# Kernel tuning notes

Measured on AMD Instinct MI355X. Metric: run time of the kernel, lower is better.

## Reference

```python
import jax, jax.numpy as jnp
import numpy as np

CURV = 0.9            # geoopt PoincareBall(0.9)
SQRT_C = CURV ** 0.5
MIN_NORM = 1e-15
PROJ_EPS = 4e-3       # geoopt float32 boundary eps
ATANH_EPS = 1e-7
COS_EPS = 1e-8        # torch.cosine_similarity eps


def _norm(x):
    return jnp.sqrt(jnp.maximum(jnp.sum(x * x, axis=-1, keepdims=True), MIN_NORM * MIN_NORM))


def _project(x):
    # project onto ball of radius (1-eps)/sqrt(c)
    n = jnp.maximum(_norm(x), MIN_NORM)
    maxnorm = (1.0 - PROJ_EPS) / SQRT_C
    return jnp.where(n > maxnorm, x / n * maxnorm, x)


def expmap0(u):
    n = jnp.maximum(_norm(u), MIN_NORM)
    gamma = jnp.tanh(SQRT_C * n) * u / (SQRT_C * n)
    return _project(gamma)


def mobius_add(x, y):
    c = CURV
    x2 = jnp.sum(x * x, axis=-1, keepdims=True)
    y2 = jnp.sum(y * y, axis=-1, keepdims=True)
    xy = jnp.sum(x * y, axis=-1, keepdims=True)
    num = (1.0 + 2.0 * c * xy + c * y2) * x + (1.0 - c * x2) * y
    den = 1.0 + 2.0 * c * xy + c * c * x2 * y2
    return num / jnp.maximum(den, MIN_NORM)


def pdist(x, y):
    # dist(x,y) = 2/sqrt(c) * artanh(sqrt(c) * ||(-x) (+) y||)
    d = mobius_add(-x, y)
    n = _norm(d)[..., 0]
    z = jnp.clip(SQRT_C * n, -1.0 + ATANH_EPS, 1.0 - ATANH_EPS)
    return 2.0 / SQRT_C * jnp.arctanh(z)


def cos_sim(a, b):
    na = jnp.maximum(jnp.sqrt(jnp.sum(a * a, axis=-1)), COS_EPS)
    nb = jnp.maximum(jnp.sqrt(jnp.sum(b * b, axis=-1)), COS_EPS)
    return jnp.sum(a * b, axis=-1) / (na * nb)


def setup_inputs() -> dict:
    key = jax.random.key(0)
    ks = jax.random.split(key, 11)
    B, L, Ls, C, Lc, H, R = 4, 512, 128, 20, 128, 768, 512
    s = 0.02  # keep projected embeddings in a realistic range
    return {
        "text_out": jax.random.normal(ks[0], (B, L, H), jnp.float32),
        "summary_out": jax.random.normal(ks[1], (B, Ls, H), jnp.float32),
        "candidate_out": jax.random.normal(ks[2], (B, C, Lc, H), jnp.float32),
        "W_d": jax.random.normal(ks[3], (H, R), jnp.float32) * s,
        "W_s": jax.random.normal(ks[4], (H, R), jnp.float32) * s,
        "W_c": jax.random.normal(ks[5], (H, R), jnp.float32) * s,
        "W_p": jax.random.normal(ks[6], (R, R), jnp.float32) * s,
        "conv_w1": jax.random.normal(ks[7], (1, H, R), jnp.float32) * s,
        "conv_b1": jax.random.normal(ks[8], (R,), jnp.float32) * s,
        "conv_w2": jax.random.normal(ks[9], (2, H, R), jnp.float32) * s,
        "conv_b2": jax.random.normal(ks[10], (R,), jnp.float32) * s,
    }


def _forward(text_out, summary_out, candidate_out, W_d, W_s, W_c, W_p,
             conv_w1, conv_b1, conv_w2, conv_b2):
    # --- document ---
    doc_emb = expmap0(text_out[:, 0, :] @ W_d)                       # [B,R]

    # NGramers (max_gram=2, eval mode so dropout is identity)
    x = text_out[:, 1:-1, :]                                         # [B,L-2,H]
    y1 = jax.nn.relu(jnp.einsum('blh,hr->blr', x, conv_w1[0]) + conv_b1)
    y2 = jax.nn.relu(jnp.einsum('blh,hr->blr', x[:, :-1], conv_w2[0])
                     + jnp.einsum('blh,hr->blr', x[:, 1:], conv_w2[1]) + conv_b2)
    gram = jnp.concatenate([y1, y2], axis=1)                         # [B,2L-5,R]

    doc_word_emb = expmap0(jnp.einsum('blr,rk->blk', gram, W_p))     # [B,T,R]
    doc_inter = 1.0 / pdist(doc_word_emb, doc_emb[:, None, :])       # [B,T]

    # --- summary ---
    summary_emb = expmap0(jnp.max(summary_out, axis=1) @ W_s)        # [B,R]
    summary_score = -pdist(summary_emb, doc_emb) ** 2                # [B]
    sum_inter = 1.0 / pdist(doc_word_emb, summary_emb[:, None, :])   # [B,T]
    summary_score = summary_score + cos_sim(doc_inter, sum_inter)    # [B]

    # --- candidates ---
    cand_emb = expmap0(jnp.einsum('bch,hr->bcr', jnp.max(candidate_out, axis=2), W_c))  # [B,C,R]
    score = -pdist(cand_emb, doc_emb[:, None, :]) ** 2               # [B,C]
    cand_inter = 1.0 / pdist(doc_word_emb[:, None, :, :], cand_emb[:, :, None, :])      # [B,C,T]
    score = score + cos_sim(doc_inter[:, None, :], cand_inter)       # [B,C]
    return score, summary_score


def reference(text_out, summary_out, candidate_out, W_d, W_s, W_c, W_p,
              conv_w1, conv_b1, conv_w2, conv_b2):
    return _forward(text_out, summary_out, candidate_out, W_d, W_s, W_c, W_p,
                    conv_w1, conv_b1, conv_w2, conv_b2)
```

## Files before the change

### kernel.cpp

```cpp
#include <hip/hip_runtime.h>
#include <math.h>

#define SQRTC  0.94868329805051381f
#define MAXN   (0.996f/SQRTC)
#define OME_CLIP (1.0f - 0.996f*0.996f)
#define TWO_OVER_SQRTC 2.1081851067789197f

typedef unsigned short u16;
typedef __attribute__((ext_vector_type(8))) short bf8;
typedef __attribute__((ext_vector_type(4))) float f4;

__device__ __forceinline__ u16 f2bf(float f){
    union { float f; unsigned int i; } v; v.f = f;
    unsigned int x = v.i;
    unsigned int lsb = (x >> 16) & 1u;
    x += 0x7fffu + lsb;
    return (u16)(x >> 16);
}
__device__ __forceinline__ float bf2f(u16 u){
    union { unsigned int i; float f; } v; v.i = ((unsigned int)u) << 16; return v.f;
}

__device__ __forceinline__ void gload16(void* lds, const void* g){
    __builtin_amdgcn_global_load_lds(
        (const __attribute__((address_space(1))) unsigned int*)g,
        (__attribute__((address_space(3))) unsigned int*)lds,
        16, 0, 0);
}

__device__ __forceinline__ float pdist_stable(float ome_x, float ome_y, float t){
    float u = 1.0f - ome_x, v = 1.0f - ome_y;
    float den = fmaxf(1.0f - 1.8f*t + u*v, 1e-15f);
    float q = ome_x*ome_y/den;
    q = fminf(fmaxf(q, 2.0e-7f), 1.0f);
    float z = sqrtf(fmaxf(1.0f - q, 0.0f));
    float at = 0.5f * logf((1.0f+z)*(1.0f+z)/q);
    return TWO_OVER_SQRTC * at;
}

__device__ __forceinline__ void expmap_scale_ome(float sum, float* fout, float* omeout){
    float nraw = sqrtf(fmaxf(sum, 1e-30f));
    float n = fmaxf(nraw, 1e-15f);
    float sn = SQRTC*n;
    float th = tanhf(sn);
    float factor = th/sn;
    float gn = factor*nraw;
    if (gn > MAXN){ *fout = factor*(MAXN/gn); *omeout = OME_CLIP; }
    else { *fout = factor; *omeout = fmaxf((1.0f-th)*(1.0f+th), 1e-12f); }
}

__global__ __launch_bounds__(256)
void k_stage1(const float* __restrict__ summ, const float* __restrict__ cand,
              const float* __restrict__ text,
              const float* __restrict__ w1, const float* __restrict__ w2,
              const float* __restrict__ wp,
              float* __restrict__ smax, float* __restrict__ cmax,
              u16* __restrict__ textb, u16* __restrict__ w1t,
              u16* __restrict__ w2t, u16* __restrict__ wpt)
{
    __shared__ float shm[1056];
    int bx = blockIdx.x;
    int t = threadIdx.x;
    if (bx < 252){
        int row = bx / 3, hc = bx - row*3;
        int w = t >> 6, lane = t & 63;
        const float* in = (row < 4) ? (summ + (long long)row*128*768)
                                    : (cand + (long long)(row-4)*128*768);
        const float* p = in + (long long)(w*32)*768 + hc*256 + lane*4;
        float4 m = make_float4(-INFINITY,-INFINITY,-INFINITY,-INFINITY);
        #pragma unroll 8
        for (int l = 0; l < 32; l++){
            float4 v = *(const float4*)(p + (long long)l*768);
            m.x = fmaxf(m.x, v.x); m.y = fmaxf(m.y, v.y);
            m.z = fmaxf(m.z, v.z); m.w = fmaxf(m.w, v.w);
        }
        float4* sm4 = (float4*)shm;
        sm4[w*64 + lane] = m; __syncthreads();
        if (t < 64){
            float4 a = sm4[t], b4 = sm4[64+t], c4 = sm4[128+t], d4 = sm4[192+t];
            float4 r;
            r.x = fmaxf(fmaxf(a.x,b4.x), fmaxf(c4.x,d4.x));
            r.y = fmaxf(fmaxf(a.y,b4.y), fmaxf(c4.y,d4.y));
            r.z = fmaxf(fmaxf(a.z,b4.z), fmaxf(c4.z,d4.z));
            r.w = fmaxf(fmaxf(a.w,b4.w), fmaxf(c4.w,d4.w));
            float* outp = (row < 4) ? (smax + row*768) : (cmax + (row-4)*768);
            *(float4*)(outp + hc*256 + t*4) = r;
        }
        return;
    }
    int pb = bx - 252;
    if (pb < 768){
        int base = pb*2048 + t*8;
        float4 a = *(const float4*)(text + base);
        float4 b = *(const float4*)(text + base + 4);
        *(ushort4*)(textb + base)     = make_ushort4(f2bf(a.x), f2bf(a.y), f2bf(a.z), f2bf(a.w));
        *(ushort4*)(textb + base + 4) = make_ushort4(f2bf(b.x), f2bf(b.y), f2bf(b.z), f2bf(b.w));
        return;
    }
    int j = pb - 768;
    const float* in; u16* outp; int K;
    if (j < 384){ in = w1; outp = w1t; K = 768; }
    else if (j < 1152){ j -= 384; in = w2; outp = w2t; K = 1536; }
    else { j -= 1152; in = wp; outp = wpt; K = 512; }
    const int N = 512, ntile = N/32;
    int k0 = (j/ntile)*32, n0 = (j - (j/ntile)*ntile)*32;
    int tx = t & 31, ty = t >> 5;
    #pragma unroll
    for (int i = 0; i < 4; i++)
        shm[(ty*4+i)*33 + tx] = in[(long long)(k0 + ty*4 + i)*N + n0 + tx];
    __syncthreads();
    #pragma unroll
    for (int i = 0; i < 4; i++)
        outp[(long long)(n0 + ty*4 + i)*K + k0 + tx] = f2bf(shm[tx*33 + ty*4+i]);
}

__global__ __launch_bounds__(256)
void k_stage2(const u16* __restrict__ textb,
              const u16* __restrict__ w1t, const u16* __restrict__ w2t,
              const float* __restrict__ cb1, const float* __restrict__ cb2,
              const float* __restrict__ text,
              const float* __restrict__ smax, const float* __restrict__ cmax,
              const float* __restrict__ W_d, const float* __restrict__ W_s,
              const float* __restrict__ W_c,
              u16* __restrict__ gram, float* __restrict__ emb_all)
{
    __shared__ char smem[16384];
    int bx = blockIdx.x;
    int t = threadIdx.x;
    if (bx < 512){
        u16* As = (u16*)smem;
        u16* Bs = (u16*)(smem + 8192);
        int xx = bx & 63, yy = bx >> 6;
        int job = xx & 1;
        int m0 = (xx >> 1) * 64;
        int n0 = yy * 64;
        int K   = job ? 1536 : 768;
        int M   = job ? 2036 : 2040;
        int rpb = job ? 509 : 510;
        int ob  = job ? 510 : 0;
        const u16* Bt = job ? w2t : w1t;
        const float* bias = job ? cb2 : cb1;

        int r0 = t >> 3;
        int co = (((t & 7) ^ (r0 & 7)) << 3);

        int gm0 = m0 + r0;      if (gm0 >= M) gm0 = M - 1;
        int gm1 = m0 + r0 + 32; if (gm1 >= M) gm1 = M - 1;
        int ab0 = gm0 / rpb, al0 = gm0 - ab0*rpb;
        int ab1 = gm1 / rpb, al1 = gm1 - ab1*rpb;
        const u16* a0 = textb + (long long)ab0*393216 + (long long)(al0+1)*768 + co;
        const u16* a1 = textb + (long long)ab1*393216 + (long long)(al1+1)*768 + co;
        const u16* bp0 = Bt + (long long)(n0 + r0)*K      + co;
        const u16* bp1 = Bt + (long long)(n0 + r0 + 32)*K + co;
        u16* lA0 = As + t*8;
        u16* lA1 = As + (256 + t)*8;
        u16* lB0 = Bs + t*8;
        u16* lB1 = Bs + (256 + t)*8;

        int lane = t & 63, wv = t >> 6;
        int fm = lane & 15, fq = lane >> 4;
        int arow = wv*16 + fm;
        int aswz = arow & 7, bswz = fm & 7;
        int aoff0 = arow*64 + ((fq     ^ aswz) << 3);
        int aoff1 = arow*64 + (((4+fq) ^ aswz) << 3);
        int boff0 = ((fq     ^ bswz) << 3);
        int boff1 = (((4+fq) ^ bswz) << 3);

        f4 acc0 = {0,0,0,0}, acc1 = {0,0,0,0}, acc2 = {0,0,0,0}, acc3 = {0,0,0,0};
        for (int k0 = 0; k0 < K; k0 += 64){
            gload16(lA0, a0 + k0);
            gload16(lA1, a1 + k0);
            gload16(lB0, bp0 + k0);
            gload16(lB1, bp1 + k0);
            __syncthreads();
            bf8 af0 = *(const bf8*)(As + aoff0);
            bf8 af1 = *(const bf8*)(As + aoff1);
            bf8 b00 = *(const bf8*)(Bs + (fm   )*64 + boff0);
            bf8 b10 = *(const bf8*)(Bs + (16+fm)*64 + boff0);
            bf8 b20 = *(const bf8*)(Bs + (32+fm)*64 + boff0);
            bf8 b30 = *(const bf8*)(Bs + (48+fm)*64 + boff0);
            bf8 b01 = *(const bf8*)(Bs + (fm   )*64 + boff1);
            bf8 b11 = *(const bf8*)(Bs + (16+fm)*64 + boff1);
            bf8 b21 = *(const bf8*)(Bs + (32+fm)*64 + boff1);
            bf8 b31 = *(const bf8*)(Bs + (48+fm)*64 + boff1);
            acc0 = __builtin_amdgcn_mfma_f32_16x16x32_bf16(af0, b00, acc0, 0, 0, 0);
            acc1 = __builtin_amdgcn_mfma_f32_16x16x32_bf16(af0, b10, acc1, 0, 0, 0);
            acc2 = __builtin_amdgcn_mfma_f32_16x16x32_bf16(af0, b20, acc2, 0, 0, 0);
            acc3 = __builtin_amdgcn_mfma_f32_16x16x32_bf16(af0, b30, acc3, 0, 0, 0);
            acc0 = __builtin_amdgcn_mfma_f32_16x16x32_bf16(af1, b01, acc0, 0, 0, 0);
            acc1 = __builtin_amdgcn_mfma_f32_16x16x32_bf16(af1, b11, acc1, 0, 0, 0);
            acc2 = __builtin_amdgcn_mfma_f32_16x16x32_bf16(af1, b21, acc2, 0, 0, 0);
            acc3 = __builtin_amdgcn_mfma_f32_16x16x32_bf16(af1, b31, acc3, 0, 0, 0);
            __syncthreads();
        }
        int col = n0 + fm;
        float bv0 = bias[col], bv1 = bias[col+16], bv2 = bias[col+32], bv3 = bias[col+48];
        #pragma unroll
        for (int i = 0; i < 4; i++){
            int row = m0 + wv*16 + fq*4 + i;
            if (row >= M) continue;
            int b = row/rpb, l = row - b*rpb;
            long long orow = (long long)b*1019 + ob + l;
            u16* gp = gram + orow*512;
            gp[col]      = f2bf(fmaxf(acc0[i] + bv0, 0.f));
            gp[col + 16] = f2bf(fmaxf(acc1[i] + bv1, 0.f));
            gp[col + 32] = f2bf(fmaxf(acc2[i] + bv2, 0.f));
            gp[col + 48] = f2bf(fmaxf(acc3[i] + bv3, 0.f));
        }
        return;
    }
    {
        int eb = bx - 512;
        int row = eb >> 3, nt = eb & 7;
        float* a   = (float*)smem;
        float* red = (float*)smem + 768;
        const float* A; const float* W;
        if (row < 4){ A = text + (long long)row*512*768; W = W_d; }
        else if (row < 8){ A = smax + (long long)(row-4)*768; W = W_s; }
        else { A = cmax + (long long)(row-8)*768; W = W_c; }
        for (int k = t; k < 768; k += 256) a[k] = A[k];
        __syncthreads();
        int lane = t & 63, kg = t >> 6;
        int col = nt*64 + lane;
        const float* Wp = W + (long long)(kg*192)*512 + col;
        float acc = 0.f;
        #pragma unroll 8
        for (int k = 0; k < 192; k++) acc += a[kg*192 + k] * Wp[k*512];
        red[t] = acc; __syncthreads();
        if (t < 64) emb_all[(long long)row*512 + col] = red[t] + red[t+64] + red[t+128] + red[t+192];
    }
}

__global__ __launch_bounds__(256)
void k_stage3(const u16* __restrict__ gram, const u16* __restrict__ wpt,
              u16* __restrict__ dwe_b,
              float* __restrict__ emb_all, float* __restrict__ ome_all,
              u16* __restrict__ emb_b)
{
    __shared__ char smem[16384];
    int bx = blockIdx.x;
    int t = threadIdx.x;
    if (bx < 512){
        u16* As = (u16*)smem;
        u16* Bs = (u16*)(smem + 8192);
        const int K = 512, M = 4076;
        int m0 = (bx >> 3) * 64;
        int n0 = (bx & 7) * 64;

        int r0 = t >> 3;
        int co = (((t & 7) ^ (r0 & 7)) << 3);
        int gm0 = m0 + r0;      if (gm0 >= M) gm0 = M - 1;
        int gm1 = m0 + r0 + 32; if (gm1 >= M) gm1 = M - 1;
        const u16* a0 = gram + (long long)gm0*512 + co;
        const u16* a1 = gram + (long long)gm1*512 + co;
        const u16* bp0 = wpt + (long long)(n0 + r0)*K      + co;
        const u16* bp1 = wpt + (long long)(n0 + r0 + 32)*K + co;
        u16* lA0 = As + t*8;
        u16* lA1 = As + (256 + t)*8;
        u16* lB0 = Bs + t*8;
        u16* lB1 = Bs + (256 + t)*8;

        int lane = t & 63, wv = t >> 6;
        int fm = lane & 15, fq = lane >> 4;
        int arow = wv*16 + fm;
        int aswz = arow & 7, bswz = fm & 7;
        int aoff0 = arow*64 + ((fq     ^ aswz) << 3);
        int aoff1 = arow*64 + (((4+fq) ^ aswz) << 3);
        int boff0 = ((fq     ^ bswz) << 3);
        int boff1 = (((4+fq) ^ bswz) << 3);

        f4 acc0 = {0,0,0,0}, acc1 = {0,0,0,0}, acc2 = {0,0,0,0}, acc3 = {0,0,0,0};
        for (int k0 = 0; k0 < K; k0 += 64){
            gload16(lA0, a0 + k0);
            gload16(lA1, a1 + k0);
            gload16(lB0, bp0 + k0);
            gload16(lB1, bp1 + k0);
            __syncthreads();
            bf8 af0 = *(const bf8*)(As + aoff0);
            bf8 af1 = *(const bf8*)(As + aoff1);
            bf8 b00 = *(const bf8*)(Bs + (fm   )*64 + boff0);
            bf8 b10 = *(const bf8*)(Bs + (16+fm)*64 + boff0);
            bf8 b20 = *(const bf8*)(Bs + (32+fm)*64 + boff0);
            bf8 b30 = *(const bf8*)(Bs + (48+fm)*64 + boff0);
            bf8 b01 = *(const bf8*)(Bs + (fm   )*64 + boff1);
            bf8 b11 = *(const bf8*)(Bs + (16+fm)*64 + boff1);
            bf8 b21 = *(const bf8*)(Bs + (32+fm)*64 + boff1);
            bf8 b31 = *(const bf8*)(Bs + (48+fm)*64 + boff1);
            acc0 = __builtin_amdgcn_mfma_f32_16x16x32_bf16(af0, b00, acc0, 0, 0, 0);
            acc1 = __builtin_amdgcn_mfma_f32_16x16x32_bf16(af0, b10, acc1, 0, 0, 0);
            acc2 = __builtin_amdgcn_mfma_f32_16x16x32_bf16(af0, b20, acc2, 0, 0, 0);
            acc3 = __builtin_amdgcn_mfma_f32_16x16x32_bf16(af0, b30, acc3, 0, 0, 0);
            acc0 = __builtin_amdgcn_mfma_f32_16x16x32_bf16(af1, b01, acc0, 0, 0, 0);
            acc1 = __builtin_amdgcn_mfma_f32_16x16x32_bf16(af1, b11, acc1, 0, 0, 0);
            acc2 = __builtin_amdgcn_mfma_f32_16x16x32_bf16(af1, b21, acc2, 0, 0, 0);
            acc3 = __builtin_amdgcn_mfma_f32_16x16x32_bf16(af1, b31, acc3, 0, 0, 0);
            __syncthreads();
        }
        int col = n0 + fm;
        #pragma unroll
        for (int i = 0; i < 4; i++){
            int row = m0 + wv*16 + fq*4 + i;
            if (row >= M) continue;
            u16* dp = dwe_b + (long long)row*512;
            dp[col]      = f2bf(acc0[i]);
            dp[col + 16] = f2bf(acc1[i]);
            dp[col + 32] = f2bf(acc2[i]);
            dp[col + 48] = f2bf(acc3[i]);
        }
        return;
    }
    {
        float* red = (float*)smem;
        int row = bx - 512;
        float* X = emb_all + (long long)row*512;
        float2 u = *(float2*)(X + t*2);
        red[t] = u.x*u.x + u.y*u.y; __syncthreads();
        for (int s = 128; s > 0; s >>= 1){ if (t < s) red[t] += red[t+s]; __syncthreads(); }
        float f, ome;
        expmap_scale_ome(red[0], &f, &ome);
        float sx = u.x*f, sy = u.y*f;
        *(float2*)(X + t*2) = make_float2(sx, sy);
        u16* Xb = emb_b + (long long)row*512;
        Xb[t*2]   = f2bf(sx);
        Xb[t*2+1] = f2bf(sy);
        if (t == 0) ome_all[row] = ome;
    }
}

__global__ __launch_bounds__(64)
void k_dots_mfma(const u16* __restrict__ dwe_b, const u16* __restrict__ emb_b,
                 const float* __restrict__ ome_all,
                 float* __restrict__ doc_inter, float* __restrict__ sum_inter,
                 float* __restrict__ cand_inter)
{
    int bx = blockIdx.x;
    int b  = bx >> 6;
    int m0 = (bx & 63) * 16;
    int t = threadIdx.x;
    int fm = t & 15, fq = t >> 4;

    int arow = m0 + fm; if (arow > 1018) arow = 1018;
    const u16* Ap = dwe_b + ((long long)(b*1019 + arow))*512 + fq*8;

    int n1 = 16 + fm; if (n1 > 21) n1 = 21;
    int e0 = (fm == 0) ? b : (fm == 1) ? 4 + b : 8 + b*20 + (fm - 2);
    int e1 = 8 + b*20 + (n1 - 2);
    const u16* B0 = emb_b + (long long)e0*512 + fq*8;
    const u16* B1 = emb_b + (long long)e1*512 + fq*8;
    float oy0 = ome_all[e0];
    float oy1 = ome_all[e1];

    f4 acc0 = {0,0,0,0}, acc1 = {0,0,0,0};
    float ssq = 0.f;
    #pragma unroll 4
    for (int k0 = 0; k0 < 512; k0 += 32){
        bf8 av  = *(const bf8*)(Ap + k0);
        bf8 bv0 = *(const bf8*)(B0 + k0);
        bf8 bv1 = *(const bf8*)(B1 + k0);
        #pragma unroll
        for (int j = 0; j < 8; j++){ float x = bf2f(((u16*)&av)[j]); ssq += x*x; }
        acc0 = __builtin_amdgcn_mfma_f32_16x16x32_bf16(av, bv0, acc0, 0, 0, 0);
        acc1 = __builtin_amdgcn_mfma_f32_16x16x32_bf16(av, bv1, acc1, 0, 0, 0);
    }
    ssq += __shfl_xor(ssq, 16);
    ssq += __shfl_xor(ssq, 32);

    #pragma unroll
    for (int i = 0; i < 4; i++){
        int r = fq*4 + i;
        float rs = __shfl(ssq, r);
        int row = m0 + r;
        if (row >= 1019) continue;
        float f, ox;
        expmap_scale_ome(rs, &f, &ox);
        long long grow = (long long)b*1019 + row;
        {
            float s = acc0[i] * f;
            float dist = pdist_stable(ox, oy0, s);
            float inv = 1.0f/fmaxf(dist, 1e-12f);
            if (fm == 0) doc_inter[grow] = inv;
            else if (fm == 1) sum_inter[grow] = inv;
            else cand_inter[((long long)(b*20 + (fm - 2)))*1019 + row] = inv;
        }
        if (16 + fm < 22){
            float s = acc1[i] * f;
            float dist = pdist_stable(ox, oy1, s);
            float inv = 1.0f/fmaxf(dist, 1e-12f);
            cand_inter[((long long)(b*20 + (16 + fm - 2)))*1019 + row] = inv;
        }
    }
}

__global__ __launch_bounds__(256)
void k_final(const float* __restrict__ doc_inter, const float* __restrict__ sum_inter,
             const float* __restrict__ cand_inter,
             const float* __restrict__ emb_all, const float* __restrict__ ome_all,
             float* __restrict__ out)
{
    __shared__ float r0[256], r1[256], r2[256], r3[256];
    int j = blockIdx.x, t = threadIdx.x;
    int b; const float *a, *bb; int xi, yi; int outIdx;
    if (j < 80){
        b = j/20;
        a  = doc_inter + b*1019;
        bb = cand_inter + (long long)j*1019;
        xi = 8 + j; yi = b;
        outIdx = j;
    } else {
        b = j - 80;
        a  = doc_inter + b*1019;
        bb = sum_inter + b*1019;
        xi = 4 + b; yi = b;
        outIdx = 80 + b;
    }
    const float* xe = emb_all + (long long)xi*512;
    const float* ye = emb_all + (long long)yi*512;
    float ox = ome_all[xi], oy = ome_all[yi];
    float saa = 0.f, sbb = 0.f, sab = 0.f, st = 0.f;
    for (int l = t; l < 1019; l += 256){ float av = a[l], bv = bb[l]; saa += av*av; sbb += bv*bv; sab += av*bv; }
    for (int k = t; k < 512; k += 256) st += xe[k]*ye[k];
    r0[t] = saa; r1[t] = sbb; r2[t] = sab; r3[t] = st; __syncthreads();
    for (int s = 128; s > 0; s >>= 1){
        if (t < s){ r0[t] += r0[t+s]; r1[t] += r1[t+s]; r2[t] += r2[t+s]; r3[t] += r3[t+s]; }
        __syncthreads();
    }
    if (t == 0){
        float na = fmaxf(sqrtf(r0[0]), 1e-8f);
        float nb = fmaxf(sqrtf(r1[0]), 1e-8f);
        float cosv = r2[0] / (na*nb);
        float pd = pdist_stable(ox, oy, r3[0]);
        out[outIdx] = -pd*pd + cosv;
    }
}

extern "C" void kernel_launch(void* const* d_in, const int* in_sizes, int n_in,
                              void* d_out, int out_size, void* d_ws, size_t ws_size,
                              hipStream_t stream) {
    const float* text = (const float*)d_in[0];
    const float* summ = (const float*)d_in[1];
    const float* cand = (const float*)d_in[2];
    const float* W_d  = (const float*)d_in[3];
    const float* W_s  = (const float*)d_in[4];
    const float* W_c  = (const float*)d_in[5];
    const float* W_p  = (const float*)d_in[6];
    const float* cw1  = (const float*)d_in[7];
    const float* cb1  = (const float*)d_in[8];
    const float* cw2  = (const float*)d_in[9];
    const float* cb2  = (const float*)d_in[10];
    float* out = (float*)d_out;

    const int B = 4, C = 20, H = 768;

    char* base = (char*)d_ws;
    size_t off = 0;
    auto allocF = [&](size_t n)->float*{ float* p = (float*)(base + off); off += ((n*4) + 255) & ~(size_t)255; return p; };
    auto allocU = [&](size_t n)->u16*{ u16* p = (u16*)(base + off); off += ((n*2) + 255) & ~(size_t)255; return p; };

    float* smax = allocF(B*H);
    float* cmax = allocF(B*C*H);
    float* emb_all = allocF(88*512);
    float* ome_all = allocF(88);
    u16* emb_b = allocU(88*512);
    u16* textb = allocU(4*512*768);
    u16* w1t   = allocU(512*768);
    u16* w2t   = allocU(512*1536);
    u16* wpt   = allocU(512*512);
    u16* gram  = allocU(4076*512);
    u16* dwe_b = allocU(4076*512);
    float* doc_inter = allocF(4076);
    float* sum_inter = allocF(4076);
    float* cand_inter= allocF(B*C*1019);

    k_stage1<<<2428, 256, 0, stream>>>(summ, cand, text, cw1, cw2, W_p,
                                       smax, cmax, textb, w1t, w2t, wpt);

    k_stage2<<<1216, 256, 0, stream>>>(textb, w1t, w2t, cb1, cb2,
                                       text, smax, cmax, W_d, W_s, W_c,
                                       gram, emb_all);

    k_stage3<<<600, 256, 0, stream>>>(gram, wpt, dwe_b, emb_all, ome_all, emb_b);

    k_dots_mfma<<<256, 64, 0, stream>>>(dwe_b, emb_b, ome_all,
                                        doc_inter, sum_inter, cand_inter);

    k_final<<<84, 256, 0, stream>>>(doc_inter, sum_inter, cand_inter,
                                    emb_all, ome_all, out);
}
```

Before: 141.4 us.

## Fuse five kernel launches into one persistent cooperative kernel with grid syncs

Replaces the five separate stage kernels with one cooperative kernel of 256 persistent blocks. Each block loops over the former per-stage block jobs, and grid-wide syncs separate the stages. This removes launch overhead and inter-kernel gaps. In exchange, occupancy is capped at one 256-thread block per CU, each block processes several jobs serially, and grid sync has its own cost.

```diff
diff --git a/kernel.cpp b/kernel.cpp
--- a/kernel.cpp
+++ b/kernel.cpp
@@ -1,5 +1,8 @@
 #include <hip/hip_runtime.h>
+#include <hip/hip_cooperative_groups.h>
 #include <math.h>
+
+namespace cg = cooperative_groups;
 
 #define SQRTC  0.94868329805051381f
 #define MAXN   (0.996f/SQRTC)
@@ -49,387 +52,373 @@
     else { *fout = factor; *omeout = fmaxf((1.0f-th)*(1.0f+th), 1e-12f); }
 }
 
-__global__ __launch_bounds__(256)
-void k_stage1(const float* __restrict__ summ, const float* __restrict__ cand,
-              const float* __restrict__ text,
-              const float* __restrict__ w1, const float* __restrict__ w2,
-              const float* __restrict__ wp,
-              float* __restrict__ smax, float* __restrict__ cmax,
-              u16* __restrict__ textb, u16* __restrict__ w1t,
-              u16* __restrict__ w2t, u16* __restrict__ wpt)
-{
-    __shared__ float shm[1056];
-    int bx = blockIdx.x;
-    int t = threadIdx.x;
-    if (bx < 252){
-        int row = bx / 3, hc = bx - row*3;
-        int w = t >> 6, lane = t & 63;
-        const float* in = (row < 4) ? (summ + (long long)row*128*768)
-                                    : (cand + (long long)(row-4)*128*768);
-        const float* p = in + (long long)(w*32)*768 + hc*256 + lane*4;
-        float4 m = make_float4(-INFINITY,-INFINITY,-INFINITY,-INFINITY);
-        #pragma unroll 8
-        for (int l = 0; l < 32; l++){
-            float4 v = *(const float4*)(p + (long long)l*768);
-            m.x = fmaxf(m.x, v.x); m.y = fmaxf(m.y, v.y);
-            m.z = fmaxf(m.z, v.z); m.w = fmaxf(m.w, v.w);
-        }
-        float4* sm4 = (float4*)shm;
-        sm4[w*64 + lane] = m; __syncthreads();
-        if (t < 64){
-            float4 a = sm4[t], b4 = sm4[64+t], c4 = sm4[128+t], d4 = sm4[192+t];
-            float4 r;
-            r.x = fmaxf(fmaxf(a.x,b4.x), fmaxf(c4.x,d4.x));
-            r.y = fmaxf(fmaxf(a.y,b4.y), fmaxf(c4.y,d4.y));
-            r.z = fmaxf(fmaxf(a.z,b4.z), fmaxf(c4.z,d4.z));
-            r.w = fmaxf(fmaxf(a.w,b4.w), fmaxf(c4.w,d4.w));
-            float* outp = (row < 4) ? (smax + row*768) : (cmax + (row-4)*768);
-            *(float4*)(outp + hc*256 + t*4) = r;
-        }
-        return;
-    }
-    int pb = bx - 252;
-    if (pb < 768){
-        int base = pb*2048 + t*8;
-        float4 a = *(const float4*)(text + base);
-        float4 b = *(const float4*)(text + base + 4);
-        *(ushort4*)(textb + base)     = make_ushort4(f2bf(a.x), f2bf(a.y), f2bf(a.z), f2bf(a.w));
-        *(ushort4*)(textb + base + 4) = make_ushort4(f2bf(b.x), f2bf(b.y), f2bf(b.z), f2bf(b.w));
-        return;
-    }
-    int j = pb - 768;
-    const float* in; u16* outp; int K;
-    if (j < 384){ in = w1; outp = w1t; K = 768; }
-    else if (j < 1152){ j -= 384; in = w2; outp = w2t; K = 1536; }
-    else { j -= 1152; in = wp; outp = wpt; K = 512; }
-    const int N = 512, ntile = N/32;
-    int k0 = (j/ntile)*32, n0 = (j - (j/ntile)*ntile)*32;
-    int tx = t & 31, ty = t >> 5;
-    #pragma unroll
-    for (int i = 0; i < 4; i++)
-        shm[(ty*4+i)*33 + tx] = in[(long long)(k0 + ty*4 + i)*N + n0 + tx];
-    __syncthreads();
-    #pragma unroll
-    for (int i = 0; i < 4; i++)
-        outp[(long long)(n0 + ty*4 + i)*K + k0 + tx] = f2bf(shm[tx*33 + ty*4+i]);
-}
-
-__global__ __launch_bounds__(256)
-void k_stage2(const u16* __restrict__ textb,
-              const u16* __restrict__ w1t, const u16* __restrict__ w2t,
-              const float* __restrict__ cb1, const float* __restrict__ cb2,
-              const float* __restrict__ text,
-              const float* __restrict__ smax, const float* __restrict__ cmax,
-              const float* __restrict__ W_d, const float* __restrict__ W_s,
-              const float* __restrict__ W_c,
-              u16* __restrict__ gram, float* __restrict__ emb_all)
+__global__ __launch_bounds__(256, 1)
+void k_mega(const float* __restrict__ summ, const float* __restrict__ cand,
+            const float* __restrict__ text,
+            const float* __restrict__ w1, const float* __restrict__ w2,
+            const float* __restrict__ wp,
+            const float* __restrict__ cb1, const float* __restrict__ cb2,
+            const float* __restrict__ W_d, const float* __restrict__ W_s,
+            const float* __restrict__ W_c,
+            float* __restrict__ smax, float* __restrict__ cmax,
+            u16* __restrict__ textb, u16* __restrict__ w1t,
+            u16* __restrict__ w2t, u16* __restrict__ wpt,
+            u16* __restrict__ gram, float* __restrict__ emb_all,
+            float* __restrict__ ome_all, u16* __restrict__ emb_b,
+            u16* __restrict__ dwe_b,
+            float* __restrict__ doc_inter, float* __restrict__ sum_inter,
+            float* __restrict__ cand_inter, float* __restrict__ out)
 {
     __shared__ char smem[16384];
-    int bx = blockIdx.x;
-    int t = threadIdx.x;
-    if (bx < 512){
-        u16* As = (u16*)smem;
-        u16* Bs = (u16*)(smem + 8192);
-        int xx = bx & 63, yy = bx >> 6;
-        int job = xx & 1;
-        int m0 = (xx >> 1) * 64;
-        int n0 = yy * 64;
-        int K   = job ? 1536 : 768;
-        int M   = job ? 2036 : 2040;
-        int rpb = job ? 509 : 510;
-        int ob  = job ? 510 : 0;
-        const u16* Bt = job ? w2t : w1t;
-        const float* bias = job ? cb2 : cb1;
-
-        int r0 = t >> 3;
-        int co = (((t & 7) ^ (r0 & 7)) << 3);
-
-        int gm0 = m0 + r0;      if (gm0 >= M) gm0 = M - 1;
-        int gm1 = m0 + r0 + 32; if (gm1 >= M) gm1 = M - 1;
-        int ab0 = gm0 / rpb, al0 = gm0 - ab0*rpb;
-        int ab1 = gm1 / rpb, al1 = gm1 - ab1*rpb;
-        const u16* a0 = textb + (long long)ab0*393216 + (long long)(al0+1)*768 + co;
-        const u16* a1 = textb + (long long)ab1*393216 + (long long)(al1+1)*768 + co;
-        const u16* bp0 = Bt + (long long)(n0 + r0)*K      + co;
-        const u16* bp1 = Bt + (long long)(n0 + r0 + 32)*K + co;
-        u16* lA0 = As + t*8;
-        u16* lA1 = As + (256 + t)*8;
-        u16* lB0 = Bs + t*8;
-        u16* lB1 = Bs + (256 + t)*8;
-
-        int lane = t & 63, wv = t >> 6;
-        int fm = lane & 15, fq = lane >> 4;
-        int arow = wv*16 + fm;
-        int aswz = arow & 7, bswz = fm & 7;
-        int aoff0 = arow*64 + ((fq     ^ aswz) << 3);
-        int aoff1 = arow*64 + (((4+fq) ^ aswz) << 3);
-        int boff0 = ((fq     ^ bswz) << 3);
-        int boff1 = (((4+fq) ^ bswz) << 3);
-
-        f4 acc0 = {0,0,0,0}, acc1 = {0,0,0,0}, acc2 = {0,0,0,0}, acc3 = {0,0,0,0};
-        for (int k0 = 0; k0 < K; k0 += 64){
-            gload16(lA0, a0 + k0);
-            gload16(lA1, a1 + k0);
-            gload16(lB0, bp0 + k0);
-            gload16(lB1, bp1 + k0);
+    cg::grid_group gg = cg::this_grid();
+    const int bx0 = blockIdx.x;
+    const int t = threadIdx.x;
+
+    for (int job = bx0; job < 2428; job += 256){
+        if (job < 252){
+            int row = job / 3, hc = job - row*3;
+            int w = t >> 6, lane = t & 63;
+            const float* in = (row < 4) ? (summ + (long long)row*128*768)
+                                        : (cand + (long long)(row-4)*128*768);
+            const float* p = in + (long long)(w*32)*768 + hc*256 + lane*4;
+            float4 m = make_float4(-INFINITY,-INFINITY,-INFINITY,-INFINITY);
+            #pragma unroll 8
+            for (int l = 0; l < 32; l++){
+                float4 v = *(const float4*)(p + (long long)l*768);
+                m.x = fmaxf(m.x, v.x); m.y = fmaxf(m.y, v.y);
+                m.z = fmaxf(m.z, v.z); m.w = fmaxf(m.w, v.w);
+            }
+            float4* sm4 = (float4*)smem;
+            sm4[w*64 + lane] = m; __syncthreads();
+            if (t < 64){
+                float4 a = sm4[t], b4 = sm4[64+t], c4 = sm4[128+t], d4 = sm4[192+t];
+                float4 r;
+                r.x = fmaxf(fmaxf(a.x,b4.x), fmaxf(c4.x,d4.x));
+                r.y = fmaxf(fmaxf(a.y,b4.y), fmaxf(c4.y,d4.y));
+                r.z = fmaxf(fmaxf(a.z,b4.z), fmaxf(c4.z,d4.z));
+                r.w = fmaxf(fmaxf(a.w,b4.w), fmaxf(c4.w,d4.w));
+                float* outp = (row < 4) ? (smax + row*768) : (cmax + (row-4)*768);
+                *(float4*)(outp + hc*256 + t*4) = r;
+            }
+        } else if (job < 1020){
+            int pb = job - 252;
+            int base = pb*2048 + t*8;
+            float4 a = *(const float4*)(text + base);
+            float4 b = *(const float4*)(text + base + 4);
+            *(ushort4*)(textb + base)     = make_ushort4(f2bf(a.x), f2bf(a.y), f2bf(a.z), f2bf(a.w));
+            *(ushort4*)(textb + base + 4) = make_ushort4(f2bf(b.x), f2bf(b.y), f2bf(b.z), f2bf(b.w));
+        } else {
+            int j = job - 1020;
+            const float* in; u16* outp; int K;
+            if (j < 384){ in = w1; outp = w1t; K = 768; }
+            else if (j < 1152){ j -= 384; in = w2; outp = w2t; K = 1536; }
+            else { j -= 1152; in = wp; outp = wpt; K = 512; }
+            const int N = 512, ntile = N/32;
+            int k0 = (j/ntile)*32, n0 = (j - (j/ntile)*ntile)*32;
+            int tx = t & 31, ty = t >> 5;
+            float* shm = (float*)smem;
+            #pragma unroll
+            for (int i = 0; i < 4; i++)
+                shm[(ty*4+i)*33 + tx] = in[(long long)(k0 + ty*4 + i)*N + n0 + tx];
             __syncthreads();
-            bf8 af0 = *(const bf8*)(As + aoff0);
-            bf8 af1 = *(const bf8*)(As + aoff1);
-            bf8 b00 = *(const bf8*)(Bs + (fm   )*64 + boff0);
-            bf8 b10 = *(const bf8*)(Bs + (16+fm)*64 + boff0);
-            bf8 b20 = *(const bf8*)(Bs + (32+fm)*64 + boff0);
-            bf8 b30 = *(const bf8*)(Bs + (48+fm)*64 + boff0);
-            bf8 b01 = *(const bf8*)(Bs + (fm   )*64 + boff1);
-            bf8 b11 = *(const bf8*)(Bs + (16+fm)*64 + boff1);
-            bf8 b21 = *(const bf8*)(Bs + (32+fm)*64 + boff1);
-            bf8 b31 = *(const bf8*)(Bs + (48+fm)*64 + boff1);
-            acc0 = __builtin_amdgcn_mfma_f32_16x16x32_bf16(af0, b00, acc0, 0, 0, 0);
-            acc1 = __builtin_amdgcn_mfma_f32_16x16x32_bf16(af0, b10, acc1, 0, 0, 0);
-            acc2 = __builtin_amdgcn_mfma_f32_16x16x32_bf16(af0, b20, acc2, 0, 0, 0);
-            acc3 = __builtin_amdgcn_mfma_f32_16x16x32_bf16(af0, b30, acc3, 0, 0, 0);
-            acc0 = __builtin_amdgcn_mfma_f32_16x16x32_bf16(af1, b01, acc0, 0, 0, 0);
-            acc1 = __builtin_amdgcn_mfma_f32_16x16x32_bf16(af1, b11, acc1, 0, 0, 0);
-            acc2 = __builtin_amdgcn_mfma_f32_16x16x32_bf16(af1, b21, acc2, 0, 0, 0);
-            acc3 = __builtin_amdgcn_mfma_f32_16x16x32_bf16(af1, b31, acc3, 0, 0, 0);
+            #pragma unroll
+            for (int i = 0; i < 4; i++)
+                outp[(long long)(n0 + ty*4 + i)*K + k0 + tx] = f2bf(shm[tx*33 + ty*4+i]);
+        }
+        __syncthreads();
+    }
+    __threadfence(); gg.sync();
+
+    for (int jr = bx0; jr < 1216; jr += 256){
+        int job = (jr >= 256 && jr < 512) ? (jr ^ 1) : jr;
+        if (job < 512){
+            u16* As = (u16*)smem;
+            u16* Bs = (u16*)(smem + 8192);
+            int xx = job & 63, yy = job >> 6;
+            int jb = xx & 1;
+            int m0 = (xx >> 1) * 64;
+            int n0 = yy * 64;
+            int K   = jb ? 1536 : 768;
+            int M   = jb ? 2036 : 2040;
+            int rpb = jb ? 509 : 510;
+            int ob  = jb ? 510 : 0;
+            const u16* Bt = jb ? w2t : w1t;
+            const float* bias = jb ? cb2 : cb1;
+
+            int r0 = t >> 3;
+            int co = (((t & 7) ^ (r0 & 7)) << 3);
+
+            int gm0 = m0 + r0;      if (gm0 >= M) gm0 = M - 1;
+            int gm1 = m0 + r0 + 32; if (gm1 >= M) gm1 = M - 1;
+            int ab0 = gm0 / rpb, al0 = gm0 - ab0*rpb;
+            int ab1 = gm1 / rpb, al1 = gm1 - ab1*rpb;
+            const u16* a0 = textb + (long long)ab0*393216 + (long long)(al0+1)*768 + co;
+            const u16* a1 = textb + (long long)ab1*393216 + (long long)(al1+1)*768 + co;
+            const u16* bp0 = Bt + (long long)(n0 + r0)*K      + co;
+            const u16* bp1 = Bt + (long long)(n0 + r0 + 32)*K + co;
+            u16* lA0 = As + t*8;
+            u16* lA1 = As + (256 + t)*8;
+            u16* lB0 = Bs + t*8;
+            u16* lB1 = Bs + (256 + t)*8;
+
+            int lane = t & 63, wv = t >> 6;
+            int fm = lane & 15, fq = lane >> 4;
+            int arow = wv*16 + fm;
+            int aswz = arow & 7, bswz = fm & 7;
+            int aoff0 = arow*64 + ((fq     ^ aswz) << 3);
+            int aoff1 = arow*64 + (((4+fq) ^ aswz) << 3);
+            int boff0 = ((fq     ^ bswz) << 3);
+            int boff1 = (((4+fq) ^ bswz) << 3);
+
+            f4 acc0 = {0,0,0,0}, acc1 = {0,0,0,0}, acc2 = {0,0,0,0}, acc3 = {0,0,0,0};
+            for (int k0 = 0; k0 < K; k0 += 64){
+                gload16(lA0, a0 + k0);
+                gload16(lA1, a1 + k0);
+                gload16(lB0, bp0 + k0);
+                gload16(lB1, bp1 + k0);
+                __syncthreads();
+                bf8 af0 = *(const bf8*)(As + aoff0);
+                bf8 af1 = *(const bf8*)(As + aoff1);
+                bf8 b00 = *(const bf8*)(Bs + (fm   )*64 + boff0);
+                bf8 b10 = *(const bf8*)(Bs + (16+fm)*64 + boff0);
+                bf8 b20 = *(const bf8*)(Bs + (32+fm)*64 + boff0);
+                bf8 b30 = *(const bf8*)(Bs + (48+fm)*64 + boff0);
+                bf8 b01 = *(const bf8*)(Bs + (fm   )*64 + boff1);
+                bf8 b11 = *(const bf8*)(Bs + (16+fm)*64 + boff1);
+                bf8 b21 = *(const bf8*)(Bs + (32+fm)*64 + boff1);
+                bf8 b31 = *(const bf8*)(Bs + (48+fm)*64 + boff1);
+                acc0 = __builtin_amdgcn_mfma_f32_16x16x32_bf16(af0, b00, acc0, 0, 0, 0);
+                acc1 = __builtin_amdgcn_mfma_f32_16x16x32_bf16(af0, b10, acc1, 0, 0, 0);
+                acc2 = __builtin_amdgcn_mfma_f32_16x16x32_bf16(af0, b20, acc2, 0, 0, 0);
+                acc3 = __builtin_amdgcn_mfma_f32_16x16x32_bf16(af0, b30, acc3, 0, 0, 0);
+                acc0 = __builtin_amdgcn_mfma_f32_16x16x32_bf16(af1, b01, acc0, 0, 0, 0);
+                acc1 = __builtin_amdgcn_mfma_f32_16x16x32_bf16(af1, b11, acc1, 0, 0, 0);
+                acc2 = __builtin_amdgcn_mfma_f32_16x16x32_bf16(af1, b21, acc2, 0, 0, 0);
+                acc3 = __builtin_amdgcn_mfma_f32_16x16x32_bf16(af1, b31, acc3, 0, 0, 0);
+                __syncthreads();
+            }
+            int col = n0 + fm;
+            float bv0 = bias[col], bv1 = bias[col+16], bv2 = bias[col+32], bv3 = bias[col+48];
+            #pragma unroll
+            for (int i = 0; i < 4; i++){
+                int row = m0 + wv*16 + fq*4 + i;
+                if (row >= M) continue;
+                int b = row/rpb, l = row - b*rpb;
+                long long orow = (long long)b*1019 + ob + l;
+                u16* gp = gram + orow*512;
+                gp[col]      = f2bf(fmaxf(acc0[i] + bv0, 0.f));
+                gp[col + 16] = f2bf(fmaxf(acc1[i] + bv1, 0.f));
+                gp[col + 32] = f2bf(fmaxf(acc2[i] + bv2, 0.f));
+                gp[col + 48] = f2bf(fmaxf(acc3[i] + bv3, 0.f));
+            }
+        } else {
+            int eb = job - 512;
+            int row = eb >> 3, nt = eb & 7;
+            float* a   = (float*)smem;
+            float* red = (float*)smem + 768;
+            const float* A; const float* W;
+            if (row < 4){ A = text + (long long)row*512*768; W = W_d; }
+            else if (row < 8){ A = smax + (long long)(row-4)*768; W = W_s; }
+            else { A = cmax + (long long)(row-8)*768; W = W_c; }
+            for (int k = t; k < 768; k += 256) a[k] = A[k];
             __syncthreads();
-        }
-        int col = n0 + fm;
-        float bv0 = bias[col], bv1 = bias[col+16], bv2 = bias[col+32], bv3 = bias[col+48];
+            int lane = t & 63, kg = t >> 6;
+            int col = nt*64 + lane;
+            const float* Wp = W + (long long)(kg*192)*512 + col;
+            float acc = 0.f;
+            #pragma unroll 8
+            for (int k = 0; k < 192; k++) acc += a[kg*192 + k] * Wp[k*512];
+            red[t] = acc; __syncthreads();
+            if (t < 64) emb_all[(long long)row*512 + col] = red[t] + red[t+64] + red[t+128] + red[t+192];
+        }
+        __syncthreads();
+    }
+    __threadfence(); gg.sync();
+
+    for (int job = bx0; job < 600; job += 256){
+        if (job < 512){
+            u16* As = (u16*)smem;
+            u16* Bs = (u16*)(smem + 8192);
+            const int K = 512, M = 4076;
+            int m0 = (job >> 3) * 64;
+            int n0 = (job & 7) * 64;
+
+            int r0 = t >> 3;
+            int co = (((t & 7) ^ (r0 & 7)) << 3);
+            int gm0 = m0 + r0;      if (gm0 >= M) gm0 = M - 1;
+            int gm1 = m0 + r0 + 32; if (gm1 >= M) gm1 = M - 1;
+            const u16* a0 = gram + (long long)gm0*512 + co;
+            const u16* a1 = gram + (long long)gm1*512 + co;
+            const u16* bp0 = wpt + (long long)(n0 + r0)*K      + co;
+            const u16* bp1 = wpt + (long long)(n0 + r0 + 32)*K + co;
+            u16* lA0 = As + t*8;
+            u16* lA1 = As + (256 + t)*8;
+            u16* lB0 = Bs + t*8;
+            u16* lB1 = Bs + (256 + t)*8;
+
+            int lane = t & 63, wv = t >> 6;
+            int fm = lane & 15, fq = lane >> 4;
+            int arow = wv*16 + fm;
+            int aswz = arow & 7, bswz = fm & 7;
+            int aoff0 = arow*64 + ((fq     ^ aswz) << 3);
+            int aoff1 = arow*64 + (((4+fq) ^ aswz) << 3);
+            int boff0 = ((fq     ^ bswz) << 3);
+            int boff1 = (((4+fq) ^ bswz) << 3);
+
+            f4 acc0 = {0,0,0,0}, acc1 = {0,0,0,0}, acc2 = {0,0,0,0}, acc3 = {0,0,0,0};
+            for (int k0 = 0; k0 < K; k0 += 64){
+                gload16(lA0, a0 + k0);
+                gload16(lA1, a1 + k0);
+                gload16(lB0, bp0 + k0);
+                gload16(lB1, bp1 + k0);
+                __syncthreads();
+                bf8 af0 = *(const bf8*)(As + aoff0);
+                bf8 af1 = *(const bf8*)(As + aoff1);
+                bf8 b00 = *(const bf8*)(Bs + (fm   )*64 + boff0);
+                bf8 b10 = *(const bf8*)(Bs + (16+fm)*64 + boff0);
+                bf8 b20 = *(const bf8*)(Bs + (32+fm)*64 + boff0);
+                bf8 b30 = *(const bf8*)(Bs + (48+fm)*64 + boff0);
+                bf8 b01 = *(const bf8*)(Bs + (fm   )*64 + boff1);
+                bf8 b11 = *(const bf8*)(Bs + (16+fm)*64 + boff1);
+                bf8 b21 = *(const bf8*)(Bs + (32+fm)*64 + boff1);
+                bf8 b31 = *(const bf8*)(Bs + (48+fm)*64 + boff1);
+                acc0 = __builtin_amdgcn_mfma_f32_16x16x32_bf16(af0, b00, acc0, 0, 0, 0);
+                acc1 = __builtin_amdgcn_mfma_f32_16x16x32_bf16(af0, b10, acc1, 0, 0, 0);
+                acc2 = __builtin_amdgcn_mfma_f32_16x16x32_bf16(af0, b20, acc2, 0, 0, 0);
+                acc3 = __builtin_amdgcn_mfma_f32_16x16x32_bf16(af0, b30, acc3, 0, 0, 0);
+                acc0 = __builtin_amdgcn_mfma_f32_16x16x32_bf16(af1, b01, acc0, 0, 0, 0);
+                acc1 = __builtin_amdgcn_mfma_f32_16x16x32_bf16(af1, b11, acc1, 0, 0, 0);
+                acc2 = __builtin_amdgcn_mfma_f32_16x16x32_bf16(af1, b21, acc2, 0, 0, 0);
+                acc3 = __builtin_amdgcn_mfma_f32_16x16x32_bf16(af1, b31, acc3, 0, 0, 0);
+                __syncthreads();
+            }
+            int col = n0 + fm;
+            #pragma unroll
+            for (int i = 0; i < 4; i++){
+                int row = m0 + wv*16 + fq*4 + i;
+                if (row >= M) continue;
+                u16* dp = dwe_b + (long long)row*512;
+                dp[col]      = f2bf(acc0[i]);
+                dp[col + 16] = f2bf(acc1[i]);
+                dp[col + 32] = f2bf(acc2[i]);
+                dp[col + 48] = f2bf(acc3[i]);
+            }
+        } else {
+            float* red = (float*)smem;
+            int row = job - 512;
+            float* X = emb_all + (long long)row*512;
+            float2 u = *(float2*)(X + t*2);
+            red[t] = u.x*u.x + u.y*u.y; __syncthreads();
+            for (int s = 128; s > 0; s >>= 1){ if (t < s) red[t] += red[t+s]; __syncthreads(); }
+            float f, ome;
+            expmap_scale_ome(red[0], &f, &ome);
+            float sx = u.x*f, sy = u.y*f;
+            *(float2*)(X + t*2) = make_float2(sx, sy);
+            u16* Xb = emb_b + (long long)row*512;
+            Xb[t*2]   = f2bf(sx);
+            Xb[t*2+1] = f2bf(sy);
+            if (t == 0) ome_all[row] = ome;
+        }
+        __syncthreads();
+    }
+    __threadfence(); gg.sync();
+
+    if (t < 64){
+        int b  = bx0 >> 6;
+        int m0 = (bx0 & 63) * 16;
+        int fm = t & 15, fq = t >> 4;
+
+        int arow = m0 + fm; if (arow > 1018) arow = 1018;
+        const u16* Ap = dwe_b + ((long long)(b*1019 + arow))*512 + fq*8;
+
+        int n1 = 16 + fm; if (n1 > 21) n1 = 21;
+        int e0 = (fm == 0) ? b : (fm == 1) ? 4 + b : 8 + b*20 + (fm - 2);
+        int e1 = 8 + b*20 + (n1 - 2);
+        const u16* B0 = emb_b + (long long)e0*512 + fq*8;
+        const u16* B1 = emb_b + (long long)e1*512 + fq*8;
+        float oy0 = ome_all[e0];
+        float oy1 = ome_all[e1];
+
+        f4 acc0 = {0,0,0,0}, acc1 = {0,0,0,0};
+        float ssq = 0.f;
+        #pragma unroll 4
+        for (int k0 = 0; k0 < 512; k0 += 32){
+            bf8 av  = *(const bf8*)(Ap + k0);
+            bf8 bv0 = *(const bf8*)(B0 + k0);
+            bf8 bv1 = *(const bf8*)(B1 + k0);
+            #pragma unroll
+            for (int j = 0; j < 8; j++){ float x = bf2f(((u16*)&av)[j]); ssq += x*x; }
+            acc0 = __builtin_amdgcn_mfma_f32_16x16x32_bf16(av, bv0, acc0, 0, 0, 0);
+            acc1 = __builtin_amdgcn_mfma_f32_16x16x32_bf16(av, bv1, acc1, 0, 0, 0);
+        }
+        ssq += __shfl_xor(ssq, 16);
+        ssq += __shfl_xor(ssq, 32);
+
         #pragma unroll
         for (int i = 0; i < 4; i++){
-            int row = m0 + wv*16 + fq*4 + i;
-            if (row >= M) continue;
-            int b = row/rpb, l = row - b*rpb;
-            long long orow = (long long)b*1019 + ob + l;
-            u16* gp = gram + orow*512;
-            gp[col]      = f2bf(fmaxf(acc0[i] + bv0, 0.f));
-            gp[col + 16] = f2bf(fmaxf(acc1[i] + bv1, 0.f));
-            gp[col + 32] = f2bf(fmaxf(acc2[i] + bv2, 0.f));
-            gp[col + 48] = f2bf(fmaxf(acc3[i] + bv3, 0.f));
-        }
-        return;
+            int r = fq*4 + i;
+            float rs = __shfl(ssq, r);
+            int row = m0 + r;
+            if (row >= 1019) continue;
+            float f, ox;
+            expmap_scale_ome(rs, &f, &ox);
+            long long grow = (long long)b*1019 + row;
+            {
+                float s = acc0[i] * f;
+                float dist = pdist_stable(ox, oy0, s);
+                float inv = 1.0f/fmaxf(dist, 1e-12f);
+                if (fm == 0) doc_inter[grow] = inv;
+                else if (fm == 1) sum_inter[grow] = inv;
+                else cand_inter[((long long)(b*20 + (fm - 2)))*1019 + row] = inv;
+            }
+            if (16 + fm < 22){
+                float s = acc1[i] * f;
+                float dist = pdist_stable(ox, oy1, s);
+                float inv = 1.0f/fmaxf(dist, 1e-12f);
+                cand_inter[((long long)(b*20 + (16 + fm - 2)))*1019 + row] = inv;
+            }
+        }
     }
-    {
-        int eb = bx - 512;
-        int row = eb >> 3, nt = eb & 7;
-        float* a   = (float*)smem;
-        float* red = (float*)smem + 768;
-        const float* A; const float* W;
-        if (row < 4){ A = text + (long long)row*512*768; W = W_d; }
-        else if (row < 8){ A = smax + (long long)(row-4)*768; W = W_s; }
-        else { A = cmax + (long long)(row-8)*768; W = W_c; }
-        for (int k = t; k < 768; k += 256) a[k] = A[k];
-        __syncthreads();
-        int lane = t & 63, kg = t >> 6;
-        int col = nt*64 + lane;
-        const float* Wp = W + (long long)(kg*192)*512 + col;
-        float acc = 0.f;
-        #pragma unroll 8
-        for (int k = 0; k < 192; k++) acc += a[kg*192 + k] * Wp[k*512];
-        red[t] = acc; __syncthreads();
-        if (t < 64) emb_all[(long long)row*512 + col] = red[t] + red[t+64] + red[t+128] + red[t+192];
-    }
-}
-
-__global__ __launch_bounds__(256)
-void k_stage3(const u16* __restrict__ gram, const u16* __restrict__ wpt,
-              u16* __restrict__ dwe_b,
-              float* __restrict__ emb_all, float* __restrict__ ome_all,
-              u16* __restrict__ emb_b)
-{
-    __shared__ char smem[16384];
-    int bx = blockIdx.x;
-    int t = threadIdx.x;
-    if (bx < 512){
-        u16* As = (u16*)smem;
-        u16* Bs = (u16*)(smem + 8192);
-        const int K = 512, M = 4076;
-        int m0 = (bx >> 3) * 64;
-        int n0 = (bx & 7) * 64;
-
-        int r0 = t >> 3;
-        int co = (((t & 7) ^ (r0 & 7)) << 3);
-        int gm0 = m0 + r0;      if (gm0 >= M) gm0 = M - 1;
-        int gm1 = m0 + r0 + 32; if (gm1 >= M) gm1 = M - 1;
-        const u16* a0 = gram + (long long)gm0*512 + co;
-        const u16* a1 = gram + (long long)gm1*512 + co;
-        const u16* bp0 = wpt + (long long)(n0 + r0)*K      + co;
-        const u16* bp1 = wpt + (long long)(n0 + r0 + 32)*K + co;
-        u16* lA0 = As + t*8;
-        u16* lA1 = As + (256 + t)*8;
-        u16* lB0 = Bs + t*8;
-        u16* lB1 = Bs + (256 + t)*8;
-
-        int lane = t & 63, wv = t >> 6;
-        int fm = lane & 15, fq = lane >> 4;
-        int arow = wv*16 + fm;
-        int aswz = arow & 7, bswz = fm & 7;
-        int aoff0 = arow*64 + ((fq     ^ aswz) << 3);
-        int aoff1 = arow*64 + (((4+fq) ^ aswz) << 3);
-        int boff0 = ((fq     ^ bswz) << 3);
-        int boff1 = (((4+fq) ^ bswz) << 3);
-
-        f4 acc0 = {0,0,0,0}, acc1 = {0,0,0,0}, acc2 = {0,0,0,0}, acc3 = {0,0,0,0};
-        for (int k0 = 0; k0 < K; k0 += 64){
-            gload16(lA0, a0 + k0);
-            gload16(lA1, a1 + k0);
-            gload16(lB0, bp0 + k0);
-            gload16(lB1, bp1 + k0);
+    __threadfence(); gg.sync();
+
+    if (bx0 < 84){
+        float* r0 = (float*)smem;
+        float* r1 = r0 + 256;
+        float* r2 = r1 + 256;
+        float* r3 = r2 + 256;
+        int j = bx0;
+        int b; const float *a, *bb; int xi, yi; int outIdx;
+        if (j < 80){
+            b = j/20;
+            a  = doc_inter + b*1019;
+            bb = cand_inter + (long long)j*1019;
+            xi = 8 + j; yi = b;
+            outIdx = j;
+        } else {
+            b = j - 80;
+            a  = doc_inter + b*1019;
+            bb = sum_inter + b*1019;
+            xi = 4 + b; yi = b;
+            outIdx = 80 + b;
+        }
+        const float* xe = emb_all + (long long)xi*512;
+        const float* ye = emb_all + (long long)yi*512;
+        float ox = ome_all[xi], oy = ome_all[yi];
+        float saa = 0.f, sbb = 0.f, sab = 0.f, st = 0.f;
+        for (int l = t; l < 1019; l += 256){ float av = a[l], bv = bb[l]; saa += av*av; sbb += bv*bv; sab += av*bv; }
+        for (int k = t; k < 512; k += 256) st += xe[k]*ye[k];
+        r0[t] = saa; r1[t] = sbb; r2[t] = sab; r3[t] = st; __syncthreads();
+        for (int s = 128; s > 0; s >>= 1){
+            if (t < s){ r0[t] += r0[t+s]; r1[t] += r1[t+s]; r2[t] += r2[t+s]; r3[t] += r3[t+s]; }
             __syncthreads();
-            bf8 af0 = *(const bf8*)(As + aoff0);
-            bf8 af1 = *(const bf8*)(As + aoff1);
-            bf8 b00 = *(const bf8*)(Bs + (fm   )*64 + boff0);
-            bf8 b10 = *(const bf8*)(Bs + (16+fm)*64 + boff0);
-            bf8 b20 = *(const bf8*)(Bs + (32+fm)*64 + boff0);
-            bf8 b30 = *(const bf8*)(Bs + (48+fm)*64 + boff0);
-            bf8 b01 = *(const bf8*)(Bs + (fm   )*64 + boff1);
-            bf8 b11 = *(const bf8*)(Bs + (16+fm)*64 + boff1);
-            bf8 b21 = *(const bf8*)(Bs + (32+fm)*64 + boff1);
-            bf8 b31 = *(const bf8*)(Bs + (48+fm)*64 + boff1);
-            acc0 = __builtin_amdgcn_mfma_f32_16x16x32_bf16(af0, b00, acc0, 0, 0, 0);
-            acc1 = __builtin_amdgcn_mfma_f32_16x16x32_bf16(af0, b10, acc1, 0, 0, 0);
-            acc2 = __builtin_amdgcn_mfma_f32_16x16x32_bf16(af0, b20, acc2, 0, 0, 0);
-            acc3 = __builtin_amdgcn_mfma_f32_16x16x32_bf16(af0, b30, acc3, 0, 0, 0);
-            acc0 = __builtin_amdgcn_mfma_f32_16x16x32_bf16(af1, b01, acc0, 0, 0, 0);
-            acc1 = __builtin_amdgcn_mfma_f32_16x16x32_bf16(af1, b11, acc1, 0, 0, 0);
-            acc2 = __builtin_amdgcn_mfma_f32_16x16x32_bf16(af1, b21, acc2, 0, 0, 0);
-            acc3 = __builtin_amdgcn_mfma_f32_16x16x32_bf16(af1, b31, acc3, 0, 0, 0);
-            __syncthreads();
-        }
-        int col = n0 + fm;
-        #pragma unroll
-        for (int i = 0; i < 4; i++){
-            int row = m0 + wv*16 + fq*4 + i;
-            if (row >= M) continue;
-            u16* dp = dwe_b + (long long)row*512;
-            dp[col]      = f2bf(acc0[i]);
-            dp[col + 16] = f2bf(acc1[i]);
-            dp[col + 32] = f2bf(acc2[i]);
-            dp[col + 48] = f2bf(acc3[i]);
-        }
-        return;
-    }
-    {
-        float* red = (float*)smem;
-        int row = bx - 512;
-        float* X = emb_all + (long long)row*512;
-        float2 u = *(float2*)(X + t*2);
-        red[t] = u.x*u.x + u.y*u.y; __syncthreads();
-        for (int s = 128; s > 0; s >>= 1){ if (t < s) red[t] += red[t+s]; __syncthreads(); }
-        float f, ome;
-        expmap_scale_ome(red[0], &f, &ome);
-        float sx = u.x*f, sy = u.y*f;
-        *(float2*)(X + t*2) = make_float2(sx, sy);
-        u16* Xb = emb_b + (long long)row*512;
-        Xb[t*2]   = f2bf(sx);
-        Xb[t*2+1] = f2bf(sy);
-        if (t == 0) ome_all[row] = ome;
-    }
-}
-
-__global__ __launch_bounds__(64)
-void k_dots_mfma(const u16* __restrict__ dwe_b, const u16* __restrict__ emb_b,
-                 const float* __restrict__ ome_all,
-                 float* __restrict__ doc_inter, float* __restrict__ sum_inter,
-                 float* __restrict__ cand_inter)
-{
-    int bx = blockIdx.x;
-    int b  = bx >> 6;
-    int m0 = (bx & 63) * 16;
-    int t = threadIdx.x;
-    int fm = t & 15, fq = t >> 4;
-
-    int arow = m0 + fm; if (arow > 1018) arow = 1018;
-    const u16* Ap = dwe_b + ((long long)(b*1019 + arow))*512 + fq*8;
-
-    int n1 = 16 + fm; if (n1 > 21) n1 = 21;
-    int e0 = (fm == 0) ? b : (fm == 1) ? 4 + b : 8 + b*20 + (fm - 2);
-    int e1 = 8 + b*20 + (n1 - 2);
-    const u16* B0 = emb_b + (long long)e0*512 + fq*8;
-    const u16* B1 = emb_b + (long long)e1*512 + fq*8;
-    float oy0 = ome_all[e0];
-    float oy1 = ome_all[e1];
-
-    f4 acc0 = {0,0,0,0}, acc1 = {0,0,0,0};
-    float ssq = 0.f;
-    #pragma unroll 4
-    for (int k0 = 0; k0 < 512; k0 += 32){
-        bf8 av  = *(const bf8*)(Ap + k0);
-        bf8 bv0 = *(const bf8*)(B0 + k0);
-        bf8 bv1 = *(const bf8*)(B1 + k0);
-        #pragma unroll
-        for (int j = 0; j < 8; j++){ float x = bf2f(((u16*)&av)[j]); ssq += x*x; }
-        acc0 = __builtin_amdgcn_mfma_f32_16x16x32_bf16(av, bv0, acc0, 0, 0, 0);
-        acc1 = __builtin_amdgcn_mfma_f32_16x16x32_bf16(av, bv1, acc1, 0, 0, 0);
-    }
-    ssq += __shfl_xor(ssq, 16);
-    ssq += __shfl_xor(ssq, 32);
-
-    #pragma unroll
-    for (int i = 0; i < 4; i++){
-        int r = fq*4 + i;
-        float rs = __shfl(ssq, r);
-        int row = m0 + r;
-        if (row >= 1019) continue;
-        float f, ox;
-        expmap_scale_ome(rs, &f, &ox);
-        long long grow = (long long)b*1019 + row;
-        {
-            float s = acc0[i] * f;
-            float dist = pdist_stable(ox, oy0, s);
-            float inv = 1.0f/fmaxf(dist, 1e-12f);
-            if (fm == 0) doc_inter[grow] = inv;
-            else if (fm == 1) sum_inter[grow] = inv;
-            else cand_inter[((long long)(b*20 + (fm - 2)))*1019 + row] = inv;
-        }
-        if (16 + fm < 22){
-            float s = acc1[i] * f;
-            float dist = pdist_stable(ox, oy1, s);
-            float inv = 1.0f/fmaxf(dist, 1e-12f);
-            cand_inter[((long long)(b*20 + (16 + fm - 2)))*1019 + row] = inv;
-        }
-    }
-}
-
-__global__ __launch_bounds__(256)
-void k_final(const float* __restrict__ doc_inter, const float* __restrict__ sum_inter,
-             const float* __restrict__ cand_inter,
-             const float* __restrict__ emb_all, const float* __restrict__ ome_all,
-             float* __restrict__ out)
-{
-    __shared__ float r0[256], r1[256], r2[256], r3[256];
-    int j = blockIdx.x, t = threadIdx.x;
-    int b; const float *a, *bb; int xi, yi; int outIdx;
-    if (j < 80){
-        b = j/20;
-        a  = doc_inter + b*1019;
-        bb = cand_inter + (long long)j*1019;
-        xi = 8 + j; yi = b;
-        outIdx = j;
-    } else {
-        b = j - 80;
-        a  = doc_inter + b*1019;
-        bb = sum_inter + b*1019;
-        xi = 4 + b; yi = b;
-        outIdx = 80 + b;
-    }
-    const float* xe = emb_all + (long long)xi*512;
-    const float* ye = emb_all + (long long)yi*512;
-    float ox = ome_all[xi], oy = ome_all[yi];
-    float saa = 0.f, sbb = 0.f, sab = 0.f, st = 0.f;
-    for (int l = t; l < 1019; l += 256){ float av = a[l], bv = bb[l]; saa += av*av; sbb += bv*bv; sab += av*bv; }
-    for (int k = t; k < 512; k += 256) st += xe[k]*ye[k];
-    r0[t] = saa; r1[t] = sbb; r2[t] = sab; r3[t] = st; __syncthreads();
-    for (int s = 128; s > 0; s >>= 1){
-        if (t < s){ r0[t] += r0[t+s]; r1[t] += r1[t+s]; r2[t] += r2[t+s]; r3[t] += r3[t+s]; }
-        __syncthreads();
-    }
-    if (t == 0){
-        float na = fmaxf(sqrtf(r0[0]), 1e-8f);
-        float nb = fmaxf(sqrtf(r1[0]), 1e-8f);
-        float cosv = r2[0] / (na*nb);
-        float pd = pdist_stable(ox, oy, r3[0]);
-        out[outIdx] = -pd*pd + cosv;
+        }
+        if (t == 0){
+            float na = fmaxf(sqrtf(r0[0]), 1e-8f);
+            float nb = fmaxf(sqrtf(r1[0]), 1e-8f);
+            float cosv = r2[0] / (na*nb);
+            float pd = pdist_stable(ox, oy, r3[0]);
+            out[outIdx] = -pd*pd + cosv;
+        }
     }
 }
 
@@ -471,18 +460,18 @@
     float* sum_inter = allocF(4076);
     float* cand_inter= allocF(B*C*1019);
 
-    k_stage1<<<2428, 256, 0, stream>>>(summ, cand, text, cw1, cw2, W_p,
-                                       smax, cmax, textb, w1t, w2t, wpt);
-
-    k_stage2<<<1216, 256, 0, stream>>>(textb, w1t, w2t, cb1, cb2,
-                                       text, smax, cmax, W_d, W_s, W_c,
-                                       gram, emb_all);
-
-    k_stage3<<<600, 256, 0, stream>>>(gram, wpt, dwe_b, emb_all, ome_all, emb_b);
-
-    k_dots_mfma<<<256, 64, 0, stream>>>(dwe_b, emb_b, ome_all,
-                                        doc_inter, sum_inter, cand_inter);
-
-    k_final<<<84, 256, 0, stream>>>(doc_inter, sum_inter, cand_inter,
-                                    emb_all, ome_all, out);
-}
+    void* args[] = {
+        (void*)&summ, (void*)&cand, (void*)&text,
+        (void*)&cw1, (void*)&cw2, (void*)&W_p,
+        (void*)&cb1, (void*)&cb2,
+        (void*)&W_d, (void*)&W_s, (void*)&W_c,
+        (void*)&smax, (void*)&cmax,
+        (void*)&textb, (void*)&w1t, (void*)&w2t, (void*)&wpt,
+        (void*)&gram, (void*)&emb_all, (void*)&ome_all, (void*)&emb_b,
+        (void*)&dwe_b,
+        (void*)&doc_inter, (void*)&sum_inter, (void*)&cand_inter,
+        (void*)&out
+    };
+    hipLaunchCooperativeKernel((const void*)k_mega, dim3(256), dim3(256),
+                               args, 0, stream);
+}
```

Result: slower. 408.0 us (+188.6%).
